# Kernel optimization log

Measured on AMD Instinct MI355X. Metric: run time of the kernel, lower is better.

Reference implementation:

```python
import jax, jax.numpy as jnp
import numpy as np

B, T, F, H, D = 4, 2048, 512, 8, 64


def setup_inputs() -> dict:
    key = jax.random.key(0)
    ks = jax.random.split(key, 12)
    s = 0.02
    inp = {
        "q": jax.random.normal(ks[0], (B, T, F), jnp.float32),
        "k": jax.random.normal(ks[1], (B, T, F), jnp.float32),
        "v": jax.random.normal(ks[2], (B, T, F), jnp.float32),
        # causal boolean mask, broadcastable to [B,H,T,T]
        "attention_mask": jnp.tril(jnp.ones((T, T), bool))[None, None],
        # projection params (EinsumDense 'btf,fhd->bthd' with bias 'hd')
        "Wq": jax.random.normal(ks[3], (F, H, D), jnp.float32) * s,
        "bq": jnp.zeros((H, D), jnp.float32),
        "Wk": jax.random.normal(ks[4], (F, H, D), jnp.float32) * s,
        "bk": jnp.zeros((H, D), jnp.float32),
        "Wv": jax.random.normal(ks[5], (F, H, D), jnp.float32) * s,
        "bv": jnp.zeros((H, D), jnp.float32),
        # relative-position params (EinsumDense 'bihd,jd->bhij' with bias 'hij')
        "R": jax.random.normal(ks[6], (T, D), jnp.float32) * s,
        "qr_bias": jnp.zeros((H, T, T), jnp.float32),
        # output projection ('bthd,hdf->btf' with bias 'f')
        "Wo": jax.random.normal(ks[7], (H, D, F), jnp.float32) * s,
        "bo": jnp.zeros((F,), jnp.float32),
    }
    return inp


def reference(q, k, v, attention_mask, Wq, bq, Wk, bk, Wv, bv, R, qr_bias, Wo, bo):
    Q = jnp.einsum("btf,fhd->bthd", q, Wq) + bq  # [B,T,H,D]
    K = jnp.einsum("btf,fhd->bthd", k, Wk) + bk
    V = jnp.einsum("btf,fhd->bthd", v, Wv) + bv
    QK = jnp.einsum("bihd,bjhd->bhij", Q, K)  # [B,H,T,T]
    QR = jnp.einsum("bihd,jd->bhij", Q, R) + qr_bias  # relative position bias
    scores = (QK + QR) / jnp.sqrt(jnp.float32(D))
    scores = jnp.where(attention_mask, scores, -1e9)
    attn = jax.nn.softmax(scores, axis=-1)
    out = jnp.einsum("bhij,bjhd->bihd", attn, V)  # [B,T,H,D]
    return jnp.einsum("bthd,hdf->btf", out, Wo) + bo  # [B,T,F]
```

## Files before the change

kernel.cpp:

```cpp
#include <hip/hip_runtime.h>
#include <hip/hip_bf16.h>
#include <stdint.h>

#define Bc 4
#define Tc 2048
#define Fc 512
#define Hc 8
#define Dc 64

typedef float  f32x4  __attribute__((ext_vector_type(4)));
typedef float  f32x16 __attribute__((ext_vector_type(16)));
typedef short  s16x8  __attribute__((ext_vector_type(8)));
typedef unsigned int   u32;
typedef unsigned int   u32x2 __attribute__((ext_vector_type(2)));
typedef unsigned int   u32x4 __attribute__((ext_vector_type(4)));
typedef unsigned short u16;
typedef unsigned short u16x4 __attribute__((ext_vector_type(4)));

static __device__ __forceinline__ u32 bfbits(float x){
  u32 u = __builtin_bit_cast(u32, x);
  return (u + 0x7fffu + ((u >> 16) & 1u)) >> 16;
}
static __device__ __forceinline__ u16 bf16o(float x){ return (u16)bfbits(x); }
static __device__ __forceinline__ float bf2f(u16 b){ u32 u = ((u32)b)<<16; return __builtin_bit_cast(float, u); }
static __device__ __forceinline__ u32 cvtpk(float lo, float hi){
  u32 r;
  asm("v_cvt_pk_bf16_f32 %0, %1, %2" : "=v"(r) : "v"(lo), "v"(hi));
  return r;
}

static __device__ __forceinline__ void plswap(u32 &a, u32 &b){
#if __has_builtin(__builtin_amdgcn_permlane32_swap)
  u32x2 r = __builtin_amdgcn_permlane32_swap(a, b, false, false);
  a = r.x; b = r.y;
#else
  u32 al = a, bl = b;
  u32 ax = (u32)__shfl_xor((int)al, 32);
  u32 bx = (u32)__shfl_xor((int)bl, 32);
  int hi = (threadIdx.x & 32) != 0;
  a = hi ? bx : al;
  b = hi ? bl : ax;
#endif
}
static __device__ __forceinline__ float halfmax(float v){
  u32 a = __builtin_bit_cast(u32, v), b = a;
  plswap(a, b);
  return fmaxf(__builtin_bit_cast(float, a), __builtin_bit_cast(float, b));
}
static __device__ __forceinline__ float halfsum(float v){
  u32 a = __builtin_bit_cast(u32, v), b = a;
  plswap(a, b);
  return __builtin_bit_cast(float, a) + __builtin_bit_cast(float, b);
}

static __device__ __forceinline__ void gload16(const void* g, void* l){
  __builtin_amdgcn_global_load_lds((const __attribute__((address_space(1))) void*)g,
                                   (__attribute__((address_space(3))) void*)l, 16, 0, 0);
}

static __device__ __forceinline__ int nchunks(int q){ return (q + 3) / 3; }

__global__ __launch_bounds__(256) void k_wtrans(const float* __restrict__ Wq, const float* __restrict__ Wk,
                                                const float* __restrict__ Wv, const float* __restrict__ Wo,
                                                u16* __restrict__ Wqt, u16* __restrict__ Wkt,
                                                u16* __restrict__ Wvt, u16* __restrict__ Wot){
  const float* s; u16* d;
  switch(blockIdx.z){ case 0: s=Wq; d=Wqt; break; case 1: s=Wk; d=Wkt; break;
                      case 2: s=Wv; d=Wvt; break; default: s=Wo; d=Wot; }
  __shared__ float tile[32][33];
  int tx = threadIdx.x & 31, ty = threadIdx.x >> 5;
  int n0 = blockIdx.x*32, k0 = blockIdx.y*32;
  #pragma unroll
  for (int i=0;i<32;i+=8) tile[ty+i][tx] = s[(size_t)(k0+ty+i)*512 + n0+tx];
  __syncthreads();
  #pragma unroll
  for (int i=0;i<32;i+=8) d[(size_t)(n0+ty+i)*512 + k0+tx] = bf16o(tile[tx][ty+i]);
}

__global__ __launch_bounds__(256) void k_gemm(
    int mode_base,
    const float* __restrict__ q32, const float* __restrict__ k32, const float* __restrict__ v32,
    const u16* __restrict__ ob,
    const u16* __restrict__ Wqt, const u16* __restrict__ Wkt, const u16* __restrict__ Wvt, const u16* __restrict__ Wot,
    const float* __restrict__ bq, const float* __restrict__ bk, const float* __restrict__ bv, const float* __restrict__ bo,
    const float* __restrict__ R,
    u16* __restrict__ Qo, u16* __restrict__ Ko, u16* __restrict__ Vto, float* __restrict__ out)
{
  const int mode = mode_base + (int)blockIdx.z;
  const float* A32 = nullptr; const u16* Bt; const float* bias;
  if      (mode==0){ A32=q32; Bt=Wqt; bias=bq; }
  else if (mode==1){ A32=k32; Bt=Wkt; bias=bk; }
  else if (mode==2){ A32=v32; Bt=Wvt; bias=bv; }
  else             {          Bt=Wot; bias=bo; }
  const int m0 = blockIdx.x*64, n0 = blockIdx.y*128;
  __shared__ alignas(16) char AsRaw[64*64*4];
  __shared__ alignas(16) u16 Bs[128*64];
  const int tid = threadIdx.x, l = tid&63, w = tid>>6;
  const int wm = (w>>1)*32, wn = (w&1)*64;
  f32x4 acc[2][4];
  #pragma unroll
  for (int i=0;i<2;i++)
    #pragma unroll
    for (int j=0;j<4;j++) acc[i][j] = (f32x4){0.f,0.f,0.f,0.f};

  for (int k0=0;k0<512;k0+=64){
    __syncthreads();
    if (mode < 3){
      #pragma unroll
      for (int i=0;i<4;i++){
        int chunk = (i*4+w)*64 + l;
        int row = chunk>>4, c = chunk&15;
        gload16(A32 + (size_t)(m0+row)*512 + k0 + c*4, AsRaw + (i*4+w)*1024);
      }
    } else {
      #pragma unroll
      for (int i=0;i<2;i++){
        int chunk = (i*4+w)*64 + l;
        int row = chunk>>3, c = chunk&7;
        gload16(ob + (size_t)(m0+row)*512 + k0 + c*8, AsRaw + (i*4+w)*1024);
      }
    }
    #pragma unroll
    for (int i=0;i<4;i++){
      int chunk = (i*4+w)*64 + l;
      int row = chunk>>3, c = chunk&7;
      gload16(Bt + (size_t)(n0+row)*512 + k0 + c*8, (char*)Bs + (i*4+w)*1024);
    }
    __syncthreads();
    #pragma unroll
    for (int kc=0;kc<2;kc++){
      s16x8 af[2], bfr[4];
      #pragma unroll
      for (int mi=0;mi<2;mi++){
        if (mode < 3){
          const float* ar = (const float*)AsRaw + (wm+mi*16+(l&15))*64 + kc*32 + (l>>4)*8;
          f32x4 a0 = *(const f32x4*)ar;
          f32x4 a1 = *(const f32x4*)(ar + 4);
          u32x4 pk4 = { cvtpk(a0[0],a0[1]), cvtpk(a0[2],a0[3]),
                        cvtpk(a1[0],a1[1]), cvtpk(a1[2],a1[3]) };
          af[mi] = __builtin_bit_cast(s16x8, pk4);
        } else {
          const u16* Ab = (const u16*)AsRaw;
          af[mi] = *(const s16x8*)&Ab[(wm+mi*16+(l&15))*64 + kc*32 + (l>>4)*8];
        }
      }
      #pragma unroll
      for (int ni=0;ni<4;ni++)
        bfr[ni] = *(const s16x8*)&Bs[(wn+ni*16+(l&15))*64 + kc*32 + (l>>4)*8];
      #pragma unroll
      for (int mi=0;mi<2;mi++)
        #pragma unroll
        for (int ni=0;ni<4;ni++)
          acc[mi][ni] = __builtin_amdgcn_mfma_f32_16x16x32_bf16(af[mi], bfr[ni], acc[mi][ni], 0,0,0);
    }
  }
  const int r0 = (l>>4)*4, cl = l&15;
  #pragma unroll
  for (int mi=0;mi<2;mi++){
    #pragma unroll
    for (int ni=0;ni<4;ni++){
      int col = n0 + wn + ni*16 + cl;
      #pragma unroll
      for (int r=0;r<4;r++){
        int row = m0 + wm + mi*16 + r0 + r;
        float val = acc[mi][ni][r] + bias[col];
        if (mode==1) val += R[(size_t)(row&2047)*64 + (col&63)];
        if (mode==0) val *= 0.18033688f;
        if (mode==3){ out[(size_t)row*512 + col] = val; }
        else {
          int b = row>>11, t = row&2047, h = col>>6, dd = col&63;
          if (mode==2) Vto[(((size_t)(b*8+h))*64 + dd)*2048 + t] = bf16o(val);
          else { u16* Dp = (mode==0)? Qo : Ko; Dp[(((size_t)(b*8+h))*2048 + t)*64 + dd] = bf16o(val); }
        }
      }
    }
  }
}

__global__ __launch_bounds__(256) void k_attn(
    const u16* __restrict__ Qb, const u16* __restrict__ Kb, const u16* __restrict__ Vtb,
    u16* __restrict__ OpA, u16* __restrict__ OpB, u16* __restrict__ OpC,
    float* __restrict__ ml)
{
  const int bid = blockIdx.x;
  const int bh = bid & 31;
  const int x = bid >> 5;
  int qt = 0, xq = 0;
  for (int q = 15; q >= 0; --q){
    int c = nchunks(q);
    if (x < xq + c){ qt = q; break; }
    xq += c;
  }
  const int ch = x - xq;
  const int tt = 2*qt + 2;
  const int jt0 = ch*6;
  int nt = tt - jt0; if (nt > 6) nt = 6;

  const int tid = threadIdx.x, l = tid&63, w = tid>>6;
  const int g5 = l>>5, li = l&31;
  const size_t base = (size_t)bh * Tc * Dc;
  const u16* Qp = Qb + base;
  const u16* Kp = Kb + base;
  const u16* Vp = Vtb + base;
  const int q0 = qt*128 + w*32;
  const int qrow = q0 + li;
  __shared__ alignas(16) char lds[32768];

  s16x8 qf[4];
  #pragma unroll
  for (int kt=0;kt<4;kt++)
    qf[kt] = *(const s16x8*)(Qp + (size_t)qrow*64 + kt*16 + g5*8);

  f32x16 oacc[2];
  #pragma unroll
  for (int dn=0;dn<2;dn++){
    #pragma unroll
    for (int i=0;i<16;i++) oacc[dn][i]=0.f;
  }
  float m = -INFINITY, lsum = 0.f;
  bool first = true;

  const int ck0 = tid, ck1 = 256 + tid;
  const int rA = ck0>>3, cA = ck0&7, rB = ck1>>3, cB = ck1&7;
  u32x4 rk[2], rv[2];

  {
    int j0 = jt0*64;
    rk[0] = *(const u32x4*)(Kp + (size_t)(j0+rA)*64 + cA*8);
    rk[1] = *(const u32x4*)(Kp + (size_t)(j0+rB)*64 + cB*8);
    rv[0] = *(const u32x4*)(Vp + (size_t)rA*Tc + j0 + cA*8);
    rv[1] = *(const u32x4*)(Vp + (size_t)rB*Tc + j0 + cB*8);
  }

  for (int t=0; t<nt; t++){
    char* Ks = lds + (t&1)*16384;
    char* Vs = Ks + 8192;
    *(u32x4*)(Ks + rA*128 + ((cA*16) ^ ((rA&7)<<4))) = rk[0];
    *(u32x4*)(Ks + rB*128 + ((cB*16) ^ ((rB&7)<<4))) = rk[1];
    *(u32x4*)(Vs + rA*128 + ((cA*16) ^ ((rA&7)<<4))) = rv[0];
    *(u32x4*)(Vs + rB*128 + ((cB*16) ^ ((rB&7)<<4))) = rv[1];
    if (t+1 < nt){
      int jn = (jt0+t+1)*64;
      rk[0] = *(const u32x4*)(Kp + (size_t)(jn+rA)*64 + cA*8);
      rk[1] = *(const u32x4*)(Kp + (size_t)(jn+rB)*64 + cB*8);
      rv[0] = *(const u32x4*)(Vp + (size_t)rA*Tc + jn + cA*8);
      rv[1] = *(const u32x4*)(Vp + (size_t)rB*Tc + jn + cB*8);
    }
    __syncthreads();

    const int j0 = (jt0+t)*64;
    const bool live = (j0 <= q0 + 31);

    if (live){
      f32x16 s[2];
      __builtin_amdgcn_s_setprio(1);
      #pragma unroll
      for (int jm=0;jm<2;jm++){
        #pragma unroll
        for (int i=0;i<16;i++) s[jm][i]=0.f;
        int rrow = jm*32 + li;
        int rs = (rrow&7)<<4;
        #pragma unroll
        for (int kt=0;kt<4;kt++){
          s16x8 kf = *(const s16x8*)(Ks + rrow*128 + (((kt*2+g5)*16) ^ rs));
          s[jm] = __builtin_amdgcn_mfma_f32_32x32x16_bf16(kf, qf[kt], s[jm], 0,0,0);
        }
      }
      __builtin_amdgcn_s_setprio(0);

      const bool needmask = (j0 + 63 > q0);
      float pm[4] = {-INFINITY,-INFINITY,-INFINITY,-INFINITY};
      #pragma unroll
      for (int jm=0;jm<2;jm++){
        #pragma unroll
        for (int r=0;r<16;r++){
          float sv = s[jm][r];
          if (needmask){
            int jl = jm*32 + (r&3) + 8*(r>>2) + 4*g5;
            sv = (j0 + jl > qrow) ? -1e30f : sv;
          }
          s[jm][r] = sv;
          pm[r&3] = fmaxf(pm[r&3], sv);
        }
      }
      float pmax = fmaxf(fmaxf(pm[0],pm[1]), fmaxf(pm[2],pm[3]));
      pmax = halfmax(pmax);
      if (first){
        m = pmax; first = false;
      } else if (!__all(pmax <= m + 11.0f)){
        float mn = fmaxf(m, pmax);
        float sc = exp2f(m - mn);
        lsum *= sc;
        #pragma unroll
        for (int r=0;r<16;r++){
          float scr = __shfl(sc, (r&3) + 8*(r>>2) + 4*g5);
          oacc[0][r] *= scr;
          oacc[1][r] *= scr;
        }
        m = mn;
      }
      float ps = 0.f;
      #pragma unroll
      for (int jm=0;jm<2;jm++)
        #pragma unroll
        for (int r=0;r<16;r++){ float e = exp2f(s[jm][r]-m); s[jm][r]=e; ps += e; }
      lsum += halfsum(ps);

      u32 pk[2][4][2];
      #pragma unroll
      for (int jm=0;jm<2;jm++)
        #pragma unroll
        for (int qq=0;qq<4;qq++)
          #pragma unroll
          for (int ww=0;ww<2;ww++)
            pk[jm][qq][ww] = cvtpk(s[jm][4*qq+2*ww], s[jm][4*qq+2*ww+1]);

      __builtin_amdgcn_s_setprio(1);
      #pragma unroll
      for (int kt2=0;kt2<4;kt2++){
        const int c2 = kt2&1, jm = kt2>>1;
        u32 e0 = pk[jm][2*c2][0], e1 = pk[jm][2*c2+1][0];
        u32 f0 = pk[jm][2*c2][1], f1 = pk[jm][2*c2+1][1];
        plswap(e0, e1);
        plswap(f0, f1);
        u32x4 fw = {e0, f0, e1, f1};
        s16x8 pf = __builtin_bit_cast(s16x8, fw);
        #pragma unroll
        for (int dn=0;dn<2;dn++){
          int vrow = dn*32 + li;
          s16x8 vf = *(const s16x8*)(Vs + vrow*128 + (((kt2*2+g5)*16) ^ ((vrow&7)<<4)));
          oacc[dn] = __builtin_amdgcn_mfma_f32_32x32x16_bf16(pf, vf, oacc[dn], 0,0,0);
        }
      }
      __builtin_amdgcn_s_setprio(0);
    }
  }

  const int slot = bh*51 + x;
  u16* Op = (slot < 1024) ? (OpA + (size_t)slot*8192)
          : (slot < 1536) ? (OpB + (size_t)(slot-1024)*8192)
                          : (OpC + (size_t)(slot-1536)*8192);
  #pragma unroll
  for (int r=0;r<16;r++){
    int ri = (r&3) + 8*(r>>2) + 4*g5;
    int row = w*32 + ri;
    Op[row*64 + li]      = bf16o(oacc[0][r]);
    Op[row*64 + 32 + li] = bf16o(oacc[1][r]);
  }
  if (l < 32){
    ml[(size_t)slot*256 + w*32 + li]       = m;
    ml[(size_t)slot*256 + 128 + w*32 + li] = lsum;
  }
}

__global__ __launch_bounds__(256) void k_comb(const u16* __restrict__ OpA, const u16* __restrict__ OpB,
                                              const u16* __restrict__ OpC, const float* __restrict__ ml,
                                              u16* __restrict__ Ob){
  const int qt = blockIdx.x, bh = blockIdx.y, h = bh&7, b = bh>>3;
  int x0 = 0;
  for (int q = 15; q > qt; --q) x0 += nchunks(q);
  const int n = nchunks(qt);
  const int tid = threadIdx.x, colp = tid&31, rbase = tid>>5;
  #pragma unroll 4
  for (int rr=0; rr<16; rr++){
    int row = rbase + rr*8;
    int trow = qt*128 + row;
    float M = -INFINITY;
    float mm[6], llv[6]; u32 vv[6];
    #pragma unroll
    for (int i=0;i<6;i++){
      if (i < n){
        int slot = bh*51 + x0 + i;
        const u16* p = (slot < 1024) ? (OpA + (size_t)slot*8192)
                     : (slot < 1536) ? (OpB + (size_t)(slot-1024)*8192)
                                     : (OpC + (size_t)(slot-1536)*8192);
        mm[i]  = ml[(size_t)slot*256 + row];
        llv[i] = ml[(size_t)slot*256 + 128 + row];
        vv[i]  = *(const u32*)(p + row*64 + colp*2);
        M = fmaxf(M, mm[i]);
      }
    }
    float L = 0.f, o0 = 0.f, o1 = 0.f;
    #pragma unroll
    for (int i=0;i<6;i++){
      if (i < n){
        float a = exp2f(mm[i] - M);
        L  += llv[i]*a;
        o0 += a*bf2f((u16)(vv[i]&0xffff));
        o1 += a*bf2f((u16)(vv[i]>>16));
      }
    }
    float r = 1.f / L;
    u32 pair = cvtpk(o0*r, o1*r);
    *(u32*)(Ob + (((size_t)b*Tc + trow)*Hc + h)*Dc + colp*2) = pair;
  }
}

extern "C" void kernel_launch(void* const* d_in, const int* in_sizes, int n_in,
                              void* d_out, int out_size, void* d_ws, size_t ws_size,
                              hipStream_t stream){
  const float* q   = (const float*)d_in[0];
  const float* k   = (const float*)d_in[1];
  const float* v   = (const float*)d_in[2];
  const float* Wq  = (const float*)d_in[4];
  const float* bq  = (const float*)d_in[5];
  const float* Wk  = (const float*)d_in[6];
  const float* bk  = (const float*)d_in[7];
  const float* Wv  = (const float*)d_in[8];
  const float* bv  = (const float*)d_in[9];
  const float* R   = (const float*)d_in[10];
  const float* Wo  = (const float*)d_in[12];
  const float* bo  = (const float*)d_in[13];
  float* out = (float*)d_out;

  char* ws = (char*)d_ws;
  const size_t SZ = (size_t)8192*512*2;
  const size_t WSZ = (size_t)512*512*2;
  u16* qb  = (u16*)(ws);
  u16* kb  = (u16*)(ws + SZ);
  u16* vb  = (u16*)(ws + 2*SZ);
  u16* Wqt = (u16*)(ws + 3*SZ);
  u16* Wkt = (u16*)(ws + 3*SZ + WSZ);
  u16* Wvt = (u16*)(ws + 3*SZ + 2*WSZ);
  u16* Wot = (u16*)(ws + 3*SZ + 3*WSZ);
  u16* Qo  = (u16*)(ws + 3*SZ + 4*WSZ);
  u16* Ko  = (u16*)(ws + 4*SZ + 4*WSZ);
  u16* Vto = (u16*)(ws + 5*SZ + 4*WSZ);
  u16* Ob  = qb;
  u16*   OpA = (u16*)d_out;
  u16*   OpB = kb;
  u16*   OpC = (u16*)((char*)vb + 0x1A0000);
  float* ml  = (float*)vb;
  if (ws_size < 6*SZ + 4*WSZ) return;

  k_wtrans<<<dim3(16,16,4), 256, 0, stream>>>(Wq,Wk,Wv,Wo,Wqt,Wkt,Wvt,Wot);
  k_gemm  <<<dim3(128,4,3), 256, 0, stream>>>(0, q,k,v,Ob, Wqt,Wkt,Wvt,Wot, bq,bk,bv,bo, R, Qo,Ko,Vto,out);
  k_attn  <<<dim3(1632),    256, 0, stream>>>(Qo,Ko,Vto,OpA,OpB,OpC,ml);
  k_comb  <<<dim3(16,32),   256, 0, stream>>>(OpA,OpB,OpC,ml,Ob);
  k_gemm  <<<dim3(128,4,1), 256, 0, stream>>>(3, q,k,v,Ob, Wqt,Wkt,Wvt,Wot, bq,bk,bv,bo, R, Qo,Ko,Vto,out);
}
```

Before: 147.7 us.

## Write single-chunk attention tiles directly to output and shrink output-proj GEMM tile

Query tiles 0-2, which need only one key chunk, now normalize by the softmax sum and write their output straight into the final O buffer. This skips the partial-result store and the combine pass for them, so the combine grid shrinks to 13 query tiles. The GEMM is templated on its M tile, and the output projection launches with 32-row tiles to double the block count. The setprio hints around the MFMA sections are also removed. Trade-offs: the output GEMM reloads the weights more often, and the direct path depends on nchunks(qt) being 1 for those tiles.

```diff
diff --git a/kernel.cpp b/kernel.cpp
--- a/kernel.cpp
+++ b/kernel.cpp
@@ -77,6 +77,7 @@
   for (int i=0;i<32;i+=8) d[(size_t)(n0+ty+i)*512 + k0+tx] = bf16o(tile[tx][ty+i]);
 }
 
+template<int BM>
 __global__ __launch_bounds__(256) void k_gemm(
     int mode_base,
     const float* __restrict__ q32, const float* __restrict__ k32, const float* __restrict__ v32,
@@ -86,20 +87,21 @@
     const float* __restrict__ R,
     u16* __restrict__ Qo, u16* __restrict__ Ko, u16* __restrict__ Vto, float* __restrict__ out)
 {
+  constexpr int MI = BM/32;
   const int mode = mode_base + (int)blockIdx.z;
   const float* A32 = nullptr; const u16* Bt; const float* bias;
   if      (mode==0){ A32=q32; Bt=Wqt; bias=bq; }
   else if (mode==1){ A32=k32; Bt=Wkt; bias=bk; }
   else if (mode==2){ A32=v32; Bt=Wvt; bias=bv; }
   else             {          Bt=Wot; bias=bo; }
-  const int m0 = blockIdx.x*64, n0 = blockIdx.y*128;
-  __shared__ alignas(16) char AsRaw[64*64*4];
+  const int m0 = blockIdx.x*BM, n0 = blockIdx.y*128;
+  __shared__ alignas(16) char AsRaw[BM*64*4];
   __shared__ alignas(16) u16 Bs[128*64];
   const int tid = threadIdx.x, l = tid&63, w = tid>>6;
-  const int wm = (w>>1)*32, wn = (w&1)*64;
-  f32x4 acc[2][4];
-  #pragma unroll
-  for (int i=0;i<2;i++)
+  const int wm = (w>>1)*(BM/2), wn = (w&1)*64;
+  f32x4 acc[MI][4];
+  #pragma unroll
+  for (int i=0;i<MI;i++)
     #pragma unroll
     for (int j=0;j<4;j++) acc[i][j] = (f32x4){0.f,0.f,0.f,0.f};
 
@@ -107,14 +109,14 @@
     __syncthreads();
     if (mode < 3){
       #pragma unroll
-      for (int i=0;i<4;i++){
+      for (int i=0;i<BM/16;i++){
         int chunk = (i*4+w)*64 + l;
         int row = chunk>>4, c = chunk&15;
         gload16(A32 + (size_t)(m0+row)*512 + k0 + c*4, AsRaw + (i*4+w)*1024);
       }
     } else {
       #pragma unroll
-      for (int i=0;i<2;i++){
+      for (int i=0;i<BM/32;i++){
         int chunk = (i*4+w)*64 + l;
         int row = chunk>>3, c = chunk&7;
         gload16(ob + (size_t)(m0+row)*512 + k0 + c*8, AsRaw + (i*4+w)*1024);
@@ -129,9 +131,9 @@
     __syncthreads();
     #pragma unroll
     for (int kc=0;kc<2;kc++){
-      s16x8 af[2], bfr[4];
-      #pragma unroll
-      for (int mi=0;mi<2;mi++){
+      s16x8 af[MI], bfr[4];
+      #pragma unroll
+      for (int mi=0;mi<MI;mi++){
         if (mode < 3){
           const float* ar = (const float*)AsRaw + (wm+mi*16+(l&15))*64 + kc*32 + (l>>4)*8;
           f32x4 a0 = *(const f32x4*)ar;
@@ -148,7 +150,7 @@
       for (int ni=0;ni<4;ni++)
         bfr[ni] = *(const s16x8*)&Bs[(wn+ni*16+(l&15))*64 + kc*32 + (l>>4)*8];
       #pragma unroll
-      for (int mi=0;mi<2;mi++)
+      for (int mi=0;mi<MI;mi++)
         #pragma unroll
         for (int ni=0;ni<4;ni++)
           acc[mi][ni] = __builtin_amdgcn_mfma_f32_16x16x32_bf16(af[mi], bfr[ni], acc[mi][ni], 0,0,0);
@@ -156,7 +158,7 @@
   }
   const int r0 = (l>>4)*4, cl = l&15;
   #pragma unroll
-  for (int mi=0;mi<2;mi++){
+  for (int mi=0;mi<MI;mi++){
     #pragma unroll
     for (int ni=0;ni<4;ni++){
       int col = n0 + wn + ni*16 + cl;
@@ -180,10 +182,10 @@
 __global__ __launch_bounds__(256) void k_attn(
     const u16* __restrict__ Qb, const u16* __restrict__ Kb, const u16* __restrict__ Vtb,
     u16* __restrict__ OpA, u16* __restrict__ OpB, u16* __restrict__ OpC,
-    float* __restrict__ ml)
+    float* __restrict__ ml, u16* __restrict__ Ob)
 {
   const int bid = blockIdx.x;
-  const int bh = bid & 31;
+  const int bh = bid & 31, h = bh & 7, b = bh >> 3;
   const int x = bid >> 5;
   int qt = 0, xq = 0;
   for (int q = 15; q >= 0; --q){
@@ -253,7 +255,6 @@
 
     if (live){
       f32x16 s[2];
-      __builtin_amdgcn_s_setprio(1);
       #pragma unroll
       for (int jm=0;jm<2;jm++){
         #pragma unroll
@@ -266,7 +267,6 @@
           s[jm] = __builtin_amdgcn_mfma_f32_32x32x16_bf16(kf, qf[kt], s[jm], 0,0,0);
         }
       }
-      __builtin_amdgcn_s_setprio(0);
 
       const bool needmask = (j0 + 63 > q0);
       float pm[4] = {-INFINITY,-INFINITY,-INFINITY,-INFINITY};
@@ -315,7 +315,6 @@
           for (int ww=0;ww<2;ww++)
             pk[jm][qq][ww] = cvtpk(s[jm][4*qq+2*ww], s[jm][4*qq+2*ww+1]);
 
-      __builtin_amdgcn_s_setprio(1);
       #pragma unroll
       for (int kt2=0;kt2<4;kt2++){
         const int c2 = kt2&1, jm = kt2>>1;
@@ -332,31 +331,43 @@
           oacc[dn] = __builtin_amdgcn_mfma_f32_32x32x16_bf16(pf, vf, oacc[dn], 0,0,0);
         }
       }
-      __builtin_amdgcn_s_setprio(0);
-    }
-  }
-
-  const int slot = bh*51 + x;
-  u16* Op = (slot < 1024) ? (OpA + (size_t)slot*8192)
-          : (slot < 1536) ? (OpB + (size_t)(slot-1024)*8192)
-                          : (OpC + (size_t)(slot-1536)*8192);
-  #pragma unroll
-  for (int r=0;r<16;r++){
-    int ri = (r&3) + 8*(r>>2) + 4*g5;
-    int row = w*32 + ri;
-    Op[row*64 + li]      = bf16o(oacc[0][r]);
-    Op[row*64 + 32 + li] = bf16o(oacc[1][r]);
-  }
-  if (l < 32){
-    ml[(size_t)slot*256 + w*32 + li]       = m;
-    ml[(size_t)slot*256 + 128 + w*32 + li] = lsum;
+    }
+  }
+
+  if (qt <= 2){
+    float rin = 1.f / lsum;
+    #pragma unroll
+    for (int r=0;r<16;r++){
+      int ri = (r&3) + 8*(r>>2) + 4*g5;
+      float rr = __shfl(rin, ri);
+      int trow = q0 + ri;
+      size_t obase = (((size_t)b*Tc + trow)*Hc + h)*Dc + li;
+      Ob[obase]      = bf16o(oacc[0][r]*rr);
+      Ob[obase + 32] = bf16o(oacc[1][r]*rr);
+    }
+  } else {
+    const int slot = bh*51 + x;
+    u16* Op = (slot < 1024) ? (OpA + (size_t)slot*8192)
+            : (slot < 1536) ? (OpB + (size_t)(slot-1024)*8192)
+                            : (OpC + (size_t)(slot-1536)*8192);
+    #pragma unroll
+    for (int r=0;r<16;r++){
+      int ri = (r&3) + 8*(r>>2) + 4*g5;
+      int row = w*32 + ri;
+      Op[row*64 + li]      = bf16o(oacc[0][r]);
+      Op[row*64 + 32 + li] = bf16o(oacc[1][r]);
+    }
+    if (l < 32){
+      ml[(size_t)slot*256 + w*32 + li]       = m;
+      ml[(size_t)slot*256 + 128 + w*32 + li] = lsum;
+    }
   }
 }
 
 __global__ __launch_bounds__(256) void k_comb(const u16* __restrict__ OpA, const u16* __restrict__ OpB,
                                               const u16* __restrict__ OpC, const float* __restrict__ ml,
                                               u16* __restrict__ Ob){
-  const int qt = blockIdx.x, bh = blockIdx.y, h = bh&7, b = bh>>3;
+  const int qt = blockIdx.x + 3, bh = blockIdx.y, h = bh&7, b = bh>>3;
   int x0 = 0;
   for (int q = 15; q > qt; --q) x0 += nchunks(q);
   const int n = nchunks(qt);
@@ -433,9 +444,9 @@
   float* ml  = (float*)vb;
   if (ws_size < 6*SZ + 4*WSZ) return;
 
-  k_wtrans<<<dim3(16,16,4), 256, 0, stream>>>(Wq,Wk,Wv,Wo,Wqt,Wkt,Wvt,Wot);
-  k_gemm  <<<dim3(128,4,3), 256, 0, stream>>>(0, q,k,v,Ob, Wqt,Wkt,Wvt,Wot, bq,bk,bv,bo, R, Qo,Ko,Vto,out);
-  k_attn  <<<dim3(1632),    256, 0, stream>>>(Qo,Ko,Vto,OpA,OpB,OpC,ml);
-  k_comb  <<<dim3(16,32),   256, 0, stream>>>(OpA,OpB,OpC,ml,Ob);
-  k_gemm  <<<dim3(128,4,1), 256, 0, stream>>>(3, q,k,v,Ob, Wqt,Wkt,Wvt,Wot, bq,bk,bv,bo, R, Qo,Ko,Vto,out);
-}
+  k_wtrans  <<<dim3(16,16,4), 256, 0, stream>>>(Wq,Wk,Wv,Wo,Wqt,Wkt,Wvt,Wot);
+  k_gemm<64><<<dim3(128,4,3), 256, 0, stream>>>(0, q,k,v,Ob, Wqt,Wkt,Wvt,Wot, bq,bk,bv,bo, R, Qo,Ko,Vto,out);
+  k_attn    <<<dim3(1632),    256, 0, stream>>>(Qo,Ko,Vto,OpA,OpB,OpC,ml,Ob);
+  k_comb    <<<dim3(13,32),   256, 0, stream>>>(OpA,OpB,OpC,ml,Ob);
+  k_gemm<32><<<dim3(256,4,1), 256, 0, stream>>>(3, q,k,v,Ob, Wqt,Wkt,Wvt,Wot, bq,bk,bv,bo, R, Qo,Ko,Vto,out);
+}
```

Result: no change. 147.9 us, median of 2 (+0.1%).
